# Performance work log

Hardware: AMD Instinct MI355X
Metric: run time of the kernel (lower is better)

Reference implementation:

```python
import jax, jax.numpy as jnp
import numpy as np

B, NK, DK, DQ, DV, H = 32, 2048, 512, 512, 512, 512


def setup_inputs() -> dict:
    key = jax.random.key(0)
    ks = jax.random.split(key, 6)
    s = 1.0 / np.sqrt(H)
    return {
        "Q": jax.random.normal(ks[0], (B, DQ), dtype=jnp.float32),
        "K": jax.random.normal(ks[1], (B, NK, DK), dtype=jnp.float32),
        "V": jax.random.normal(ks[2], (B, NK, DV), dtype=jnp.float32),
        "Wk": jax.random.normal(ks[3], (DK, H), dtype=jnp.float32) * s,
        "bk": jnp.zeros((H,), dtype=jnp.float32),
        "Wq": jax.random.normal(ks[4], (DQ, H), dtype=jnp.float32) * s,
        "bq": jnp.zeros((H,), dtype=jnp.float32),
        "Wh": jax.random.normal(ks[5], (H, 1), dtype=jnp.float32) * s,
        "bh": jnp.zeros((1,), dtype=jnp.float32),
    }


def reference(Q, K, V, Wk, bk, Wq, bq, Wh, bh):
    # tk: [B, NK, H]; tq: [B, 1, H] broadcasts over n_keys (dropout_p=0 -> identity)
    tk = jnp.einsum("bnk,kh->bnh", K, Wk) + bk
    tq = (Q @ Wq + bq)[:, None, :]
    # energies: [B, NK, 1] -> relu -> softmax over n_keys (dim=1)
    energies = jax.nn.relu(jnp.einsum("bnh,ho->bno", tk + tq, Wh) + bh)
    weights = jax.nn.softmax(energies, axis=1)          # [B, NK, 1]
    output = jnp.einsum("bno,bnv->bv", weights, V)      # squeezed bmm
    return output, weights[..., 0]
```

## Files before the change

kernel.cpp:

```cpp
#include <hip/hip_runtime.h>

#define NB    32
#define NKEYS 2048
#define DKH   512
#define NCHUNK 32
#define ROWS_PER_CHUNK (NKEYS / NCHUNK)

__device__ __forceinline__ float wave_sum(float v) {
    #pragma unroll
    for (int o = 32; o > 0; o >>= 1) v += __shfl_xor(v, o);
    return v;
}
__device__ __forceinline__ float wave_max(float v) {
    #pragma unroll
    for (int o = 32; o > 0; o >>= 1) v = fmaxf(v, __shfl_xor(v, o));
    return v;
}

__global__ void prep_w_kernel(const float* __restrict__ Wk, const float* __restrict__ Wq,
                              const float* __restrict__ Wh,
                              float* __restrict__ wkh, float* __restrict__ wqh) {
    int dk = blockIdx.x;
    int lane = threadIdx.x;
    float sk = 0.f, sq = 0.f;
    #pragma unroll
    for (int h = lane; h < DKH; h += 64) {
        float wh = Wh[h];
        sk = fmaf(Wk[dk * DKH + h], wh, sk);
        sq = fmaf(Wq[dk * DKH + h], wh, sq);
    }
    sk = wave_sum(sk);
    sq = wave_sum(sq);
    if (lane == 0) { wkh[dk] = sk; wqh[dk] = sq; }
}

__global__ void prep_q_kernel(const float* __restrict__ Q, const float* __restrict__ bk,
                              const float* __restrict__ bq, const float* __restrict__ bh,
                              const float* __restrict__ Wh, const float* __restrict__ wqh,
                              float* __restrict__ qdot) {
    int b = blockIdx.x;
    int lane = threadIdx.x;
    float s = 0.f;
    #pragma unroll
    for (int h = lane; h < DKH; h += 64) s = fmaf(bk[h] + bq[h], Wh[h], s);
    #pragma unroll
    for (int d = lane; d < DKH; d += 64) s = fmaf(Q[b * DKH + d], wqh[d], s);
    s = wave_sum(s);
    if (lane == 0) qdot[b] = s + bh[0];
}

__global__ __launch_bounds__(256) void energy_kernel(const float* __restrict__ K,
        const float* __restrict__ wkh, const float* __restrict__ qdot,
        float* __restrict__ e) {
    int tid  = threadIdx.x;
    int lane = tid & 63, wv = tid >> 6;
    long row = (long)blockIdx.x * 4 + wv;
    int b = (int)(row >> 11);
    const float4* kr = (const float4*)(K + row * DKH);
    const float4* wr = (const float4*)wkh;
    float4 k0 = kr[lane],      w0 = wr[lane];
    float4 k1 = kr[lane + 64], w1 = wr[lane + 64];
    float s = k0.x * w0.x + k0.y * w0.y + k0.z * w0.z + k0.w * w0.w;
    s += k1.x * w1.x + k1.y * w1.y + k1.z * w1.z + k1.w * w1.w;
    s = wave_sum(s);
    if (lane == 0) e[row] = fmaxf(s + qdot[b], 0.f);
}

__global__ __launch_bounds__(256) void softmax_kernel(const float* __restrict__ e,
        float* __restrict__ wout) {
    int b = blockIdx.x, tid = threadIdx.x;
    int lane = tid & 63, wv = tid >> 6;
    const float4* er = (const float4*)(e + b * NKEYS);
    float4 v0 = er[tid], v1 = er[tid + 256];

    __shared__ float sred[4];
    float m = fmaxf(fmaxf(fmaxf(v0.x, v0.y), fmaxf(v0.z, v0.w)),
                    fmaxf(fmaxf(v1.x, v1.y), fmaxf(v1.z, v1.w)));
    m = wave_max(m);
    if (lane == 0) sred[wv] = m;
    __syncthreads();
    m = fmaxf(fmaxf(sred[0], sred[1]), fmaxf(sred[2], sred[3]));
    __syncthreads();

    float4 p0, p1;
    p0.x = expf(v0.x - m); p0.y = expf(v0.y - m);
    p0.z = expf(v0.z - m); p0.w = expf(v0.w - m);
    p1.x = expf(v1.x - m); p1.y = expf(v1.y - m);
    p1.z = expf(v1.z - m); p1.w = expf(v1.w - m);
    float s = p0.x + p0.y + p0.z + p0.w + p1.x + p1.y + p1.z + p1.w;
    s = wave_sum(s);
    if (lane == 0) sred[wv] = s;
    __syncthreads();
    s = sred[0] + sred[1] + sred[2] + sred[3];
    float inv = 1.f / s;

    float4* wo = (float4*)(wout + b * NKEYS);
    p0.x *= inv; p0.y *= inv; p0.z *= inv; p0.w *= inv;
    p1.x *= inv; p1.y *= inv; p1.z *= inv; p1.w *= inv;
    wo[tid] = p0;
    wo[tid + 256] = p1;
}

__global__ __launch_bounds__(256) void weightedv_kernel(const float* __restrict__ V,
        const float* __restrict__ w, float* __restrict__ partial) {
    int chunk = blockIdx.x & (NCHUNK - 1);
    int b     = blockIdx.x >> 5;
    int tid   = threadIdx.x;
    int n0    = chunk * ROWS_PER_CHUNK;
    const float2* vb = (const float2*)(V + ((long)b * NKEYS + n0) * DKH);
    const float*  wb = w + b * NKEYS + n0;
    float2 acc = {0.f, 0.f};
    #pragma unroll 4
    for (int r = 0; r < ROWS_PER_CHUNK; ++r) {
        float wt = wb[r];
        float2 vv = vb[r * (DKH / 2) + tid];
        acc.x = fmaf(wt, vv.x, acc.x);
        acc.y = fmaf(wt, vv.y, acc.y);
    }
    ((float2*)(partial + ((long)(b * NCHUNK + chunk)) * DKH))[tid] = acc;
}

__global__ void reduce_kernel(const float* __restrict__ partial, float* __restrict__ out) {
    int i = blockIdx.x * 256 + threadIdx.x;
    int b = i >> 9;
    int v = i & 511;
    float s = 0.f;
    #pragma unroll
    for (int c = 0; c < NCHUNK; ++c) s += partial[(long)((b * NCHUNK + c) << 9) + v];
    out[i] = s;
}

extern "C" void kernel_launch(void* const* d_in, const int* in_sizes, int n_in,
                              void* d_out, int out_size, void* d_ws, size_t ws_size,
                              hipStream_t stream) {
    const float* Q  = (const float*)d_in[0];
    const float* K  = (const float*)d_in[1];
    const float* V  = (const float*)d_in[2];
    const float* Wk = (const float*)d_in[3];
    const float* bk = (const float*)d_in[4];
    const float* Wq = (const float*)d_in[5];
    const float* bq = (const float*)d_in[6];
    const float* Wh = (const float*)d_in[7];
    const float* bh = (const float*)d_in[8];

    float* out  = (float*)d_out;
    float* wout = out + NB * DKH;

    float* ws      = (float*)d_ws;
    float* wkh     = ws;
    float* wqh     = ws + 512;
    float* qdot    = ws + 1024;
    float* e       = ws + 2048;
    float* partial = ws + 2048 + NB * NKEYS;

    prep_w_kernel<<<DKH, 64, 0, stream>>>(Wk, Wq, Wh, wkh, wqh);
    prep_q_kernel<<<NB, 64, 0, stream>>>(Q, bk, bq, bh, Wh, wqh, qdot);
    energy_kernel<<<(NB * NKEYS) / 4, 256, 0, stream>>>(K, wkh, qdot, e);
    softmax_kernel<<<NB, 256, 0, stream>>>(e, wout);
    weightedv_kernel<<<NB * NCHUNK, 256, 0, stream>>>(V, wout, partial);
    reduce_kernel<<<(NB * DKH) / 256, 256, 0, stream>>>(partial, out);
}
```

Measured before the change: 62.43 us.

## Fuse energy, chunked online softmax and weighted-V into one kernel with finalize pass

Replaces six kernels with three. Energy computation, a per-chunk softmax (local max and sum) and the weighted V accumulation run in one kernel per 64-row chunk, and a finalize kernel rescales the chunk partials and the weights using flash-style max/sum correction. The two prep kernels are merged into one launch, and the query term now computes Q@Wq per output column instead of folding Wq with Wh first, which is more arithmetic per batch block. This removes launch overhead and the round trips of the energies and weights through global memory, at the cost of a slower, serial-ish per-batch query projection loop.

After: 77.72 us. +24.5%, slower.

```diff
diff --git a/kernel.cpp b/kernel.cpp
--- a/kernel.cpp
+++ b/kernel.cpp
@@ -1,10 +1,10 @@
 #include <hip/hip_runtime.h>
 
-#define NB    32
-#define NKEYS 2048
-#define DKH   512
+#define NB     32
+#define NKEYS  2048
+#define D      512
 #define NCHUNK 32
-#define ROWS_PER_CHUNK (NKEYS / NCHUNK)
+#define RPC    (NKEYS / NCHUNK)
 
 __device__ __forceinline__ float wave_sum(float v) {
     #pragma unroll
@@ -17,117 +17,130 @@
     return v;
 }
 
-__global__ void prep_w_kernel(const float* __restrict__ Wk, const float* __restrict__ Wq,
-                              const float* __restrict__ Wh,
-                              float* __restrict__ wkh, float* __restrict__ wqh) {
-    int dk = blockIdx.x;
-    int lane = threadIdx.x;
-    float sk = 0.f, sq = 0.f;
-    #pragma unroll
-    for (int h = lane; h < DKH; h += 64) {
-        float wh = Wh[h];
-        sk = fmaf(Wk[dk * DKH + h], wh, sk);
-        sq = fmaf(Wq[dk * DKH + h], wh, sq);
+__global__ __launch_bounds__(256) void prep_kernel(const float* __restrict__ Wk,
+        const float* __restrict__ Wq, const float* __restrict__ Wh,
+        const float* __restrict__ Q, const float* __restrict__ bk,
+        const float* __restrict__ bq, const float* __restrict__ bh,
+        float* __restrict__ wkh, float* __restrict__ qdot) {
+    int tid = threadIdx.x, lane = tid & 63, wv = tid >> 6;
+    __shared__ float sred[4];
+    if (blockIdx.x < D) {
+        int dk = blockIdx.x;
+        float s = 0.f;
+        #pragma unroll
+        for (int h = tid; h < D; h += 256) s = fmaf(Wk[dk * D + h], Wh[h], s);
+        s = wave_sum(s);
+        if (lane == 0) sred[wv] = s;
+        __syncthreads();
+        if (tid == 0) wkh[dk] = sred[0] + sred[1] + sred[2] + sred[3];
+    } else {
+        int b = blockIdx.x - D;
+        __shared__ float sh_q[D];
+        #pragma unroll
+        for (int d = tid; d < D; d += 256) sh_q[d] = Q[b * D + d];
+        __syncthreads();
+        float acc = 0.f;
+        #pragma unroll
+        for (int hh = 0; hh < 2; ++hh) {
+            int h = tid + hh * 256;
+            float th = 0.f;
+            for (int d = 0; d < D; ++d) th = fmaf(sh_q[d], Wq[d * D + h], th);
+            acc = fmaf(th + bk[h] + bq[h], Wh[h], acc);
+        }
+        acc = wave_sum(acc);
+        if (lane == 0) sred[wv] = acc;
+        __syncthreads();
+        if (tid == 0) qdot[b] = sred[0] + sred[1] + sred[2] + sred[3] + bh[0];
     }
-    sk = wave_sum(sk);
-    sq = wave_sum(sq);
-    if (lane == 0) { wkh[dk] = sk; wqh[dk] = sq; }
 }
 
-__global__ void prep_q_kernel(const float* __restrict__ Q, const float* __restrict__ bk,
-                              const float* __restrict__ bq, const float* __restrict__ bh,
-                              const float* __restrict__ Wh, const float* __restrict__ wqh,
-                              float* __restrict__ qdot) {
-    int b = blockIdx.x;
-    int lane = threadIdx.x;
-    float s = 0.f;
-    #pragma unroll
-    for (int h = lane; h < DKH; h += 64) s = fmaf(bk[h] + bq[h], Wh[h], s);
-    #pragma unroll
-    for (int d = lane; d < DKH; d += 64) s = fmaf(Q[b * DKH + d], wqh[d], s);
-    s = wave_sum(s);
-    if (lane == 0) qdot[b] = s + bh[0];
-}
+__global__ __launch_bounds__(256) void fused_kernel(const float* __restrict__ K,
+        const float* __restrict__ V, const float* __restrict__ wkh,
+        const float* __restrict__ qdot, float* __restrict__ p_out,
+        float* __restrict__ mc_out, float* __restrict__ sc_out,
+        float* __restrict__ y_out) {
+    int chunk = blockIdx.x & (NCHUNK - 1);
+    int b     = blockIdx.x >> 5;
+    int tid = threadIdx.x, lane = tid & 63, wv = tid >> 6;
+    long base = (long)b * NKEYS + chunk * RPC;
+    __shared__ float sh[RPC];
 
-__global__ __launch_bounds__(256) void energy_kernel(const float* __restrict__ K,
-        const float* __restrict__ wkh, const float* __restrict__ qdot,
-        float* __restrict__ e) {
-    int tid  = threadIdx.x;
-    int lane = tid & 63, wv = tid >> 6;
-    long row = (long)blockIdx.x * 4 + wv;
-    int b = (int)(row >> 11);
-    const float4* kr = (const float4*)(K + row * DKH);
     const float4* wr = (const float4*)wkh;
-    float4 k0 = kr[lane],      w0 = wr[lane];
-    float4 k1 = kr[lane + 64], w1 = wr[lane + 64];
-    float s = k0.x * w0.x + k0.y * w0.y + k0.z * w0.z + k0.w * w0.w;
-    s += k1.x * w1.x + k1.y * w1.y + k1.z * w1.z + k1.w * w1.w;
-    s = wave_sum(s);
-    if (lane == 0) e[row] = fmaxf(s + qdot[b], 0.f);
-}
+    float4 w0 = wr[lane], w1 = wr[lane + 64];
+    float qd = qdot[b];
 
-__global__ __launch_bounds__(256) void softmax_kernel(const float* __restrict__ e,
-        float* __restrict__ wout) {
-    int b = blockIdx.x, tid = threadIdx.x;
-    int lane = tid & 63, wv = tid >> 6;
-    const float4* er = (const float4*)(e + b * NKEYS);
-    float4 v0 = er[tid], v1 = er[tid + 256];
-
-    __shared__ float sred[4];
-    float m = fmaxf(fmaxf(fmaxf(v0.x, v0.y), fmaxf(v0.z, v0.w)),
-                    fmaxf(fmaxf(v1.x, v1.y), fmaxf(v1.z, v1.w)));
-    m = wave_max(m);
-    if (lane == 0) sred[wv] = m;
-    __syncthreads();
-    m = fmaxf(fmaxf(sred[0], sred[1]), fmaxf(sred[2], sred[3]));
+    #pragma unroll 4
+    for (int r = wv * 16; r < wv * 16 + 16; ++r) {
+        const float4* kr = (const float4*)(K + (base + r) * D);
+        float4 k0 = kr[lane], k1 = kr[lane + 64];
+        float s = k0.x * w0.x + k0.y * w0.y + k0.z * w0.z + k0.w * w0.w
+                + k1.x * w1.x + k1.y * w1.y + k1.z * w1.z + k1.w * w1.w;
+        s = wave_sum(s);
+        if (lane == 0) sh[r] = fmaxf(s + qd, 0.f);
+    }
     __syncthreads();
 
-    float4 p0, p1;
-    p0.x = expf(v0.x - m); p0.y = expf(v0.y - m);
-    p0.z = expf(v0.z - m); p0.w = expf(v0.w - m);
-    p1.x = expf(v1.x - m); p1.y = expf(v1.y - m);
-    p1.z = expf(v1.z - m); p1.w = expf(v1.w - m);
-    float s = p0.x + p0.y + p0.z + p0.w + p1.x + p1.y + p1.z + p1.w;
-    s = wave_sum(s);
-    if (lane == 0) sred[wv] = s;
+    if (wv == 0) {
+        float e = sh[lane];
+        float m = wave_max(e);
+        float pv = expf(e - m);
+        sh[lane] = pv;
+        p_out[base + lane] = pv;
+        float ssum = wave_sum(pv);
+        if (lane == 0) { mc_out[b * NCHUNK + chunk] = m; sc_out[b * NCHUNK + chunk] = ssum; }
+    }
     __syncthreads();
-    s = sred[0] + sred[1] + sred[2] + sred[3];
-    float inv = 1.f / s;
 
-    float4* wo = (float4*)(wout + b * NKEYS);
-    p0.x *= inv; p0.y *= inv; p0.z *= inv; p0.w *= inv;
-    p1.x *= inv; p1.y *= inv; p1.z *= inv; p1.w *= inv;
-    wo[tid] = p0;
-    wo[tid + 256] = p1;
-}
-
-__global__ __launch_bounds__(256) void weightedv_kernel(const float* __restrict__ V,
-        const float* __restrict__ w, float* __restrict__ partial) {
-    int chunk = blockIdx.x & (NCHUNK - 1);
-    int b     = blockIdx.x >> 5;
-    int tid   = threadIdx.x;
-    int n0    = chunk * ROWS_PER_CHUNK;
-    const float2* vb = (const float2*)(V + ((long)b * NKEYS + n0) * DKH);
-    const float*  wb = w + b * NKEYS + n0;
+    const float2* vb = (const float2*)(V + base * D);
     float2 acc = {0.f, 0.f};
     #pragma unroll 4
-    for (int r = 0; r < ROWS_PER_CHUNK; ++r) {
-        float wt = wb[r];
-        float2 vv = vb[r * (DKH / 2) + tid];
+    for (int r = 0; r < RPC; ++r) {
+        float wt = sh[r];
+        float2 vv = vb[r * (D / 2) + tid];
         acc.x = fmaf(wt, vv.x, acc.x);
         acc.y = fmaf(wt, vv.y, acc.y);
     }
-    ((float2*)(partial + ((long)(b * NCHUNK + chunk)) * DKH))[tid] = acc;
+    ((float2*)(y_out + ((long)(b * NCHUNK + chunk)) * D))[tid] = acc;
 }
 
-__global__ void reduce_kernel(const float* __restrict__ partial, float* __restrict__ out) {
-    int i = blockIdx.x * 256 + threadIdx.x;
-    int b = i >> 9;
-    int v = i & 511;
-    float s = 0.f;
+__global__ __launch_bounds__(256) void finalize_kernel(const float* __restrict__ p,
+        const float* __restrict__ mc, const float* __restrict__ sc,
+        const float* __restrict__ y, float* __restrict__ out,
+        float* __restrict__ wout) {
+    int b = blockIdx.x, tid = threadIdx.x;
+    __shared__ float sh_f[NCHUNK];
+    if (tid < NCHUNK) {
+        float m_c = mc[b * NCHUNK + tid];
+        float s_c = sc[b * NCHUNK + tid];
+        float m = m_c;
+        #pragma unroll
+        for (int o = 16; o > 0; o >>= 1) m = fmaxf(m, __shfl_xor(m, o));
+        float ex = expf(m_c - m);
+        float S = s_c * ex;
+        #pragma unroll
+        for (int o = 1; o < 32; o <<= 1) S += __shfl_xor(S, o);
+        sh_f[tid] = ex / S;
+    }
+    __syncthreads();
+
+    const float* pb = p + b * NKEYS;
+    float* wb = wout + b * NKEYS;
     #pragma unroll
-    for (int c = 0; c < NCHUNK; ++c) s += partial[(long)((b * NCHUNK + c) << 9) + v];
-    out[i] = s;
+    for (int i = 0; i < 8; ++i) {
+        int n = tid + i * 256;
+        wb[n] = pb[n] * sh_f[n >> 6];
+    }
+
+    float2 acc = {0.f, 0.f};
+    const float2* yb = (const float2*)(y + (long)b * NCHUNK * D);
+    #pragma unroll
+    for (int c = 0; c < NCHUNK; ++c) {
+        float f = sh_f[c];
+        float2 vv = yb[c * (D / 2) + tid];
+        acc.x = fmaf(f, vv.x, acc.x);
+        acc.y = fmaf(f, vv.y, acc.y);
+    }
+    ((float2*)(out + b * D))[tid] = acc;
 }
 
 extern "C" void kernel_launch(void* const* d_in, const int* in_sizes, int n_in,
@@ -144,19 +157,17 @@
     const float* bh = (const float*)d_in[8];
 
     float* out  = (float*)d_out;
-    float* wout = out + NB * DKH;
+    float* wout = out + NB * D;
 
-    float* ws      = (float*)d_ws;
-    float* wkh     = ws;
-    float* wqh     = ws + 512;
-    float* qdot    = ws + 1024;
-    float* e       = ws + 2048;
-    float* partial = ws + 2048 + NB * NKEYS;
+    float* ws   = (float*)d_ws;
+    float* wkh  = ws;
+    float* qdot = ws + 512;
+    float* pbuf = ws + 1024;
+    float* mc   = pbuf + NB * NKEYS;
+    float* sc   = mc + NB * NCHUNK;
+    float* ybuf = sc + NB * NCHUNK;
 
-    prep_w_kernel<<<DKH, 64, 0, stream>>>(Wk, Wq, Wh, wkh, wqh);
-    prep_q_kernel<<<NB, 64, 0, stream>>>(Q, bk, bq, bh, Wh, wqh, qdot);
-    energy_kernel<<<(NB * NKEYS) / 4, 256, 0, stream>>>(K, wkh, qdot, e);
-    softmax_kernel<<<NB, 256, 0, stream>>>(e, wout);
-    weightedv_kernel<<<NB * NCHUNK, 256, 0, stream>>>(V, wout, partial);
-    reduce_kernel<<<(NB * DKH) / 256, 256, 0, stream>>>(partial, out);
+    prep_kernel<<<D + NB, 256, 0, stream>>>(Wk, Wq, Wh, Q, bk, bq, bh, wkh, qdot);
+    fused_kernel<<<NB * NCHUNK, 256, 0, stream>>>(K, V, wkh, qdot, pbuf, mc, sc, ybuf);
+    finalize_kernel<<<NB, 256, 0, stream>>>(pbuf, mc, sc, ybuf, out, wout);
 }
```

## Fuse energy, exp and weighted-V into one pass without max subtraction

Applied to the files above, without the earlier changes.

Merges the energy, softmax and weighted-V kernels into a single kernel in which each wave handles 8 key rows. It computes exp(relu(e)) without subtracting the max, writes unnormalised weights and partial V sums, and a finalize kernel normalises both. The goal is to remove the separate launches and the round trips of energies and weights through memory, so K and V are read in one sweep. The cost is a larger partial buffer (256 partial sums per batch) to reduce, and an overflow risk, since without the max shift a large positive energy can overflow exp.

Result: slower. 67.14 us (+7.5%).

```diff
diff --git a/kernel.cpp b/kernel.cpp
--- a/kernel.cpp
+++ b/kernel.cpp
@@ -2,132 +2,132 @@
 
 #define NB    32
 #define NKEYS 2048
-#define DKH   512
-#define NCHUNK 32
-#define ROWS_PER_CHUNK (NKEYS / NCHUNK)
+#define D     512
+#define RPW   8
+#define SUBS  (NKEYS / RPW)
+#define NWAVE (NB * SUBS)
 
 __device__ __forceinline__ float wave_sum(float v) {
     #pragma unroll
     for (int o = 32; o > 0; o >>= 1) v += __shfl_xor(v, o);
     return v;
 }
-__device__ __forceinline__ float wave_max(float v) {
-    #pragma unroll
-    for (int o = 32; o > 0; o >>= 1) v = fmaxf(v, __shfl_xor(v, o));
-    return v;
+
+__global__ __launch_bounds__(256) void prep_kernel(const float* __restrict__ Wk,
+        const float* __restrict__ Wq, const float* __restrict__ Wh,
+        const float* __restrict__ bk, const float* __restrict__ bq,
+        const float* __restrict__ bh,
+        float* __restrict__ wkh, float* __restrict__ wqh, float* __restrict__ cbias) {
+    int tid = threadIdx.x, lane = tid & 63, wv = tid >> 6;
+    __shared__ float sred[8];
+    if (blockIdx.x < D) {
+        int dk = blockIdx.x;
+        float sk = 0.f, sq = 0.f;
+        #pragma unroll
+        for (int h = tid; h < D; h += 256) {
+            float wh = Wh[h];
+            sk = fmaf(Wk[dk * D + h], wh, sk);
+            sq = fmaf(Wq[dk * D + h], wh, sq);
+        }
+        sk = wave_sum(sk); sq = wave_sum(sq);
+        if (lane == 0) { sred[wv] = sk; sred[wv + 4] = sq; }
+        __syncthreads();
+        if (tid == 0) wkh[dk] = sred[0] + sred[1] + sred[2] + sred[3];
+        if (tid == 1) wqh[dk] = sred[4] + sred[5] + sred[6] + sred[7];
+    } else {
+        float s = 0.f;
+        #pragma unroll
+        for (int h = tid; h < D; h += 256) s = fmaf(bk[h] + bq[h], Wh[h], s);
+        s = wave_sum(s);
+        if (lane == 0) sred[wv] = s;
+        __syncthreads();
+        if (tid == 0) cbias[0] = sred[0] + sred[1] + sred[2] + sred[3] + bh[0];
+    }
 }
 
-__global__ void prep_w_kernel(const float* __restrict__ Wk, const float* __restrict__ Wq,
-                              const float* __restrict__ Wh,
-                              float* __restrict__ wkh, float* __restrict__ wqh) {
-    int dk = blockIdx.x;
-    int lane = threadIdx.x;
-    float sk = 0.f, sq = 0.f;
+__global__ __launch_bounds__(256, 4) void mega_kernel(const float* __restrict__ K,
+        const float* __restrict__ V, const float* __restrict__ Q,
+        const float* __restrict__ wkh, const float* __restrict__ wqh,
+        const float* __restrict__ cbias,
+        float* __restrict__ p_out, float* __restrict__ partial) {
+    int tid = threadIdx.x, lane = tid & 63, wv = tid >> 6;
+    int gw = blockIdx.x * 4 + wv;
+    int b  = gw >> 8;
+    long rowbase = (long)b * NKEYS + (gw & (SUBS - 1)) * RPW;
+
+    const float4* wk4 = (const float4*)wkh;
+    float4 wa = wk4[lane], wb = wk4[lane + 64];
+
+    const float4* q4  = (const float4*)(Q + b * D);
+    const float4* wq4 = (const float4*)wqh;
+    float4 qa = q4[lane], qb = q4[lane + 64];
+    float4 xa = wq4[lane], xb = wq4[lane + 64];
+    float qd = qa.x * xa.x + qa.y * xa.y + qa.z * xa.z + qa.w * xa.w
+             + qb.x * xb.x + qb.y * xb.y + qb.z * xb.z + qb.w * xb.w;
+    qd = wave_sum(qd) + cbias[0];
+
+    float p[RPW];
     #pragma unroll
-    for (int h = lane; h < DKH; h += 64) {
-        float wh = Wh[h];
-        sk = fmaf(Wk[dk * DKH + h], wh, sk);
-        sq = fmaf(Wq[dk * DKH + h], wh, sq);
+    for (int r = 0; r < RPW; ++r) {
+        const float4* kr = (const float4*)(K + (rowbase + r) * D);
+        float4 ka = kr[lane], kb = kr[lane + 64];
+        float s = ka.x * wa.x + ka.y * wa.y + ka.z * wa.z + ka.w * wa.w
+                + kb.x * wb.x + kb.y * wb.y + kb.z * wb.z + kb.w * wb.w;
+        s = wave_sum(s);
+        p[r] = expf(fmaxf(s + qd, 0.f));
     }
-    sk = wave_sum(sk);
-    sq = wave_sum(sq);
-    if (lane == 0) { wkh[dk] = sk; wqh[dk] = sq; }
+
+    float pst = p[0];
+    #pragma unroll
+    for (int r = 1; r < RPW; ++r) if (lane == r) pst = p[r];
+    if (lane < RPW) p_out[rowbase + lane] = pst;
+
+    float4 ya = {0.f, 0.f, 0.f, 0.f}, yb = {0.f, 0.f, 0.f, 0.f};
+    #pragma unroll
+    for (int r = 0; r < RPW; ++r) {
+        const float4* vr = (const float4*)(V + (rowbase + r) * D);
+        float4 va = vr[lane], vb4 = vr[lane + 64];
+        float w = p[r];
+        ya.x = fmaf(w, va.x, ya.x);  ya.y = fmaf(w, va.y, ya.y);
+        ya.z = fmaf(w, va.z, ya.z);  ya.w = fmaf(w, va.w, ya.w);
+        yb.x = fmaf(w, vb4.x, yb.x); yb.y = fmaf(w, vb4.y, yb.y);
+        yb.z = fmaf(w, vb4.z, yb.z); yb.w = fmaf(w, vb4.w, yb.w);
+    }
+    float4* po = (float4*)(partial + (long)gw * D);
+    po[lane]      = ya;
+    po[lane + 64] = yb;
 }
 
-__global__ void prep_q_kernel(const float* __restrict__ Q, const float* __restrict__ bk,
-                              const float* __restrict__ bq, const float* __restrict__ bh,
-                              const float* __restrict__ Wh, const float* __restrict__ wqh,
-                              float* __restrict__ qdot) {
-    int b = blockIdx.x;
-    int lane = threadIdx.x;
+__global__ __launch_bounds__(256) void finalize_kernel(const float* __restrict__ p,
+        const float* __restrict__ partial, float* __restrict__ out,
+        float* __restrict__ wout) {
+    int b = blockIdx.x >> 1, half = blockIdx.x & 1;
+    int tid = threadIdx.x, lane = tid & 63, wv = tid >> 6;
+
+    const float4* p4 = (const float4*)(p + b * NKEYS);
     float s = 0.f;
     #pragma unroll
-    for (int h = lane; h < DKH; h += 64) s = fmaf(bk[h] + bq[h], Wh[h], s);
-    #pragma unroll
-    for (int d = lane; d < DKH; d += 64) s = fmaf(Q[b * DKH + d], wqh[d], s);
+    for (int i = 0; i < 2; ++i) {
+        float4 v = p4[tid + i * 256];
+        s += v.x + v.y + v.z + v.w;
+    }
     s = wave_sum(s);
-    if (lane == 0) qdot[b] = s + bh[0];
-}
-
-__global__ __launch_bounds__(256) void energy_kernel(const float* __restrict__ K,
-        const float* __restrict__ wkh, const float* __restrict__ qdot,
-        float* __restrict__ e) {
-    int tid  = threadIdx.x;
-    int lane = tid & 63, wv = tid >> 6;
-    long row = (long)blockIdx.x * 4 + wv;
-    int b = (int)(row >> 11);
-    const float4* kr = (const float4*)(K + row * DKH);
-    const float4* wr = (const float4*)wkh;
-    float4 k0 = kr[lane],      w0 = wr[lane];
-    float4 k1 = kr[lane + 64], w1 = wr[lane + 64];
-    float s = k0.x * w0.x + k0.y * w0.y + k0.z * w0.z + k0.w * w0.w;
-    s += k1.x * w1.x + k1.y * w1.y + k1.z * w1.z + k1.w * w1.w;
-    s = wave_sum(s);
-    if (lane == 0) e[row] = fmaxf(s + qdot[b], 0.f);
-}
-
-__global__ __launch_bounds__(256) void softmax_kernel(const float* __restrict__ e,
-        float* __restrict__ wout) {
-    int b = blockIdx.x, tid = threadIdx.x;
-    int lane = tid & 63, wv = tid >> 6;
-    const float4* er = (const float4*)(e + b * NKEYS);
-    float4 v0 = er[tid], v1 = er[tid + 256];
-
     __shared__ float sred[4];
-    float m = fmaxf(fmaxf(fmaxf(v0.x, v0.y), fmaxf(v0.z, v0.w)),
-                    fmaxf(fmaxf(v1.x, v1.y), fmaxf(v1.z, v1.w)));
-    m = wave_max(m);
-    if (lane == 0) sred[wv] = m;
-    __syncthreads();
-    m = fmaxf(fmaxf(sred[0], sred[1]), fmaxf(sred[2], sred[3]));
-    __syncthreads();
-
-    float4 p0, p1;
-    p0.x = expf(v0.x - m); p0.y = expf(v0.y - m);
-    p0.z = expf(v0.z - m); p0.w = expf(v0.w - m);
-    p1.x = expf(v1.x - m); p1.y = expf(v1.y - m);
-    p1.z = expf(v1.z - m); p1.w = expf(v1.w - m);
-    float s = p0.x + p0.y + p0.z + p0.w + p1.x + p1.y + p1.z + p1.w;
-    s = wave_sum(s);
     if (lane == 0) sred[wv] = s;
     __syncthreads();
-    s = sred[0] + sred[1] + sred[2] + sred[3];
-    float inv = 1.f / s;
+    float inv = 1.f / (sred[0] + sred[1] + sred[2] + sred[3]);
 
-    float4* wo = (float4*)(wout + b * NKEYS);
-    p0.x *= inv; p0.y *= inv; p0.z *= inv; p0.w *= inv;
-    p1.x *= inv; p1.y *= inv; p1.z *= inv; p1.w *= inv;
-    wo[tid] = p0;
-    wo[tid + 256] = p1;
-}
+    const float* pb = p + b * NKEYS + half * 1024;
+    float* wb = wout + b * NKEYS + half * 1024;
+    #pragma unroll
+    for (int i = 0; i < 4; ++i) wb[tid + i * 256] = pb[tid + i * 256] * inv;
 
-__global__ __launch_bounds__(256) void weightedv_kernel(const float* __restrict__ V,
-        const float* __restrict__ w, float* __restrict__ partial) {
-    int chunk = blockIdx.x & (NCHUNK - 1);
-    int b     = blockIdx.x >> 5;
-    int tid   = threadIdx.x;
-    int n0    = chunk * ROWS_PER_CHUNK;
-    const float2* vb = (const float2*)(V + ((long)b * NKEYS + n0) * DKH);
-    const float*  wb = w + b * NKEYS + n0;
-    float2 acc = {0.f, 0.f};
-    #pragma unroll 4
-    for (int r = 0; r < ROWS_PER_CHUNK; ++r) {
-        float wt = wb[r];
-        float2 vv = vb[r * (DKH / 2) + tid];
-        acc.x = fmaf(wt, vv.x, acc.x);
-        acc.y = fmaf(wt, vv.y, acc.y);
-    }
-    ((float2*)(partial + ((long)(b * NCHUNK + chunk)) * DKH))[tid] = acc;
-}
-
-__global__ void reduce_kernel(const float* __restrict__ partial, float* __restrict__ out) {
-    int i = blockIdx.x * 256 + threadIdx.x;
-    int b = i >> 9;
-    int v = i & 511;
-    float s = 0.f;
-    #pragma unroll
-    for (int c = 0; c < NCHUNK; ++c) s += partial[(long)((b * NCHUNK + c) << 9) + v];
-    out[i] = s;
+    int v = half * 256 + tid;
+    const float* pp = partial + (long)b * SUBS * D + v;
+    float acc = 0.f;
+    #pragma unroll 8
+    for (int sc = 0; sc < SUBS; ++sc) acc += pp[(long)sc * D];
+    out[b * D + v] = acc * inv;
 }
 
 extern "C" void kernel_launch(void* const* d_in, const int* in_sizes, int n_in,
@@ -144,19 +144,16 @@
     const float* bh = (const float*)d_in[8];
 
     float* out  = (float*)d_out;
-    float* wout = out + NB * DKH;
+    float* wout = out + NB * D;
 
     float* ws      = (float*)d_ws;
     float* wkh     = ws;
     float* wqh     = ws + 512;
-    float* qdot    = ws + 1024;
-    float* e       = ws + 2048;
-    float* partial = ws + 2048 + NB * NKEYS;
+    float* cbias   = ws + 1024;
+    float* pbuf    = ws + 1088;
+    float* partial = pbuf + NB * NKEYS;
 
-    prep_w_kernel<<<DKH, 64, 0, stream>>>(Wk, Wq, Wh, wkh, wqh);
-    prep_q_kernel<<<NB, 64, 0, stream>>>(Q, bk, bq, bh, Wh, wqh, qdot);
-    energy_kernel<<<(NB * NKEYS) / 4, 256, 0, stream>>>(K, wkh, qdot, e);
-    softmax_kernel<<<NB, 256, 0, stream>>>(e, wout);
-    weightedv_kernel<<<NB * NCHUNK, 256, 0, stream>>>(V, wout, partial);
-    reduce_kernel<<<(NB * DKH) / 256, 256, 0, stream>>>(partial, out);
+    prep_kernel<<<D + 1, 256, 0, stream>>>(Wk, Wq, Wh, bk, bq, bh, wkh, wqh, cbias);
+    mega_kernel<<<NWAVE / 4, 256, 0, stream>>>(K, V, Q, wkh, wqh, cbias, pbuf, partial);
+    finalize_kernel<<<NB * 2, 256, 0, stream>>>(pbuf, partial, out, wout);
 }
```
